# Kernel optimization log

Hardware: AMD Instinct MI355X
Metric: run time of the kernel (lower is better)

## Reference

```python
import jax, jax.numpy as jnp
import numpy as np

MIN_EXPERT_CAPACITY = 4
EPS = 1e-9
CAPACITY_FACTOR = 2.0  # eval capacity factor


def cumsum_exclusive(t, axis):
    return jnp.cumsum(t, axis=axis) - t


def safe_one_hot(idx, depth):
    # one_hot with an extra slot so idx == depth maps to nothing, then slice
    return jax.nn.one_hot(idx, depth + 1)[..., :depth]


def setup_inputs() -> dict:
    key = jax.random.key(0)
    k_x, k_g, k_w1, k_w2 = jax.random.split(key, 4)
    b, n, d, e, h = 2, 4096, 512, 16, 2048
    x = jax.random.normal(k_x, (b, n, d), dtype=jnp.float32)
    w_gating = jax.random.normal(k_g, (d, e), dtype=jnp.float32) / np.sqrt(d)
    w1 = jax.random.normal(k_w1, (e, d, h), dtype=jnp.float32) / np.sqrt(d)
    w2 = jax.random.normal(k_w2, (e, h, d), dtype=jnp.float32) / np.sqrt(h)
    return {"x": x, "w_gating": w_gating, "w1": w1, "w2": w2}


def top2_gating(x, w_gating):
    b, n, d = x.shape
    e = w_gating.shape[-1]
    raw_gates = jax.nn.softmax(jnp.einsum('bnd,de->bne', x, w_gating), axis=-1)

    gate_1 = jnp.max(raw_gates, axis=-1)
    index_1 = jnp.argmax(raw_gates, axis=-1)
    mask_1 = jax.nn.one_hot(index_1, e, dtype=raw_gates.dtype)

    gates_without_top1 = raw_gates * (1.0 - mask_1)
    gate_2 = jnp.max(gates_without_top1, axis=-1)
    index_2 = jnp.argmax(gates_without_top1, axis=-1)
    mask_2 = jax.nn.one_hot(index_2, e, dtype=raw_gates.dtype)

    denom = gate_1 + gate_2 + EPS
    gate_1 = gate_1 / denom
    gate_2 = gate_2 / denom

    # load-balancing loss
    density_1 = jnp.mean(mask_1, axis=-2)
    density_1_proxy = jnp.mean(raw_gates, axis=-2)
    loss = jnp.mean(density_1_proxy * density_1) * float(e * e)

    # second policy == 'all' -> keep mask_2 as-is

    capacity = max(min(n, int((n * 2) * CAPACITY_FACTOR / e)), MIN_EXPERT_CAPACITY)
    cap_f = float(capacity)

    pos1 = cumsum_exclusive(mask_1, axis=-2) * mask_1  # [b,n,e]
    mask_1 = mask_1 * (pos1 < cap_f).astype(mask_1.dtype)
    mask_1_count = jnp.sum(mask_1, axis=-2, keepdims=True)
    mask_1_flat = jnp.sum(mask_1, axis=-1)  # [b,n]
    pos1 = jnp.sum(pos1, axis=-1)
    gate_1 = gate_1 * mask_1_flat

    pos2 = (cumsum_exclusive(mask_2, axis=-2) + mask_1_count) * mask_2
    mask_2 = mask_2 * (pos2 < cap_f).astype(mask_2.dtype)
    mask_2_flat = jnp.sum(mask_2, axis=-1)
    pos2 = jnp.sum(pos2, axis=-1)
    gate_2 = gate_2 * mask_2_flat

    # combine tensor: [b, n, e, c]
    combine = (gate_1[..., None, None] * mask_1_flat[..., None, None]
               * jax.nn.one_hot(index_1, e, dtype=x.dtype)[..., None]
               * safe_one_hot(pos1.astype(jnp.int32), capacity)[..., None, :]
               + gate_2[..., None, None] * mask_2_flat[..., None, None]
               * jax.nn.one_hot(index_2, e, dtype=x.dtype)[..., None]
               * safe_one_hot(pos2.astype(jnp.int32), capacity)[..., None, :])
    dispatch = (combine > 0).astype(combine.dtype)
    return dispatch, combine, loss


def reference(x, w_gating, w1, w2):
    dispatch, combine, loss = top2_gating(x, w_gating)
    # dispatch: gather tokens into expert buckets [e, b, c, d]
    expert_inputs = jnp.einsum('bnd,bnec->ebcd', x, dispatch)
    # expert FFN (eval mode: dropout is identity)
    hidden = jax.nn.relu(jnp.einsum('ebcd,edh->ebch', expert_inputs, w1))
    expert_outputs = jnp.einsum('ebch,ehd->ebcd', hidden, w2)
    # combine back to token order, weighted by gate values
    output = jnp.einsum('ebcd,bnec->bnd', expert_outputs, combine)
    return output
```

## Files before the change

### kernel.cpp

```cpp
#include <hip/hip_runtime.h>

#define BB 2
#define NN 4096
#define DD 512
#define EE 16
#define HH 2048
#define CAP 1024
#define NTOK (BB*NN)
#define MM (BB*CAP)
#define MAXSTRIP 160

typedef unsigned short ushort_t;
typedef __attribute__((ext_vector_type(8))) short bf16x8;
typedef __attribute__((ext_vector_type(4))) float floatx4;

__device__ __forceinline__ ushort_t f2bf(float f) {
    union { float f; unsigned u; } v; v.f = f;
    unsigned r = v.u + 0x7fffu + ((v.u >> 16) & 1u);
    return (ushort_t)(r >> 16);
}

__device__ __forceinline__ void cp16(const void* g, void* l) {
    __builtin_amdgcn_global_load_lds(
        (const __attribute__((address_space(1))) void*)g,
        (__attribute__((address_space(3))) void*)l, 16, 0, 0);
}

__launch_bounds__(256)
__global__ void gating_kernel(const float* __restrict__ x,
                              const float* __restrict__ wg,
                              int* __restrict__ e1, int* __restrict__ e2,
                              float* __restrict__ g1, float* __restrict__ g2,
                              ushort_t* __restrict__ xbf) {
    int wave = threadIdx.x >> 6;
    int lane = threadIdx.x & 63;
    int t = blockIdx.x * 4 + wave;
    const float* xp = x + (size_t)t * DD;

    float4 xa = ((const float4*)xp)[lane * 2];
    float4 xb = ((const float4*)xp)[lane * 2 + 1];
    float xs[8] = {xa.x, xa.y, xa.z, xa.w, xb.x, xb.y, xb.z, xb.w};

    ushort4 h0, h1;
    h0.x = f2bf(xs[0]); h0.y = f2bf(xs[1]); h0.z = f2bf(xs[2]); h0.w = f2bf(xs[3]);
    h1.x = f2bf(xs[4]); h1.y = f2bf(xs[5]); h1.z = f2bf(xs[6]); h1.w = f2bf(xs[7]);
    ushort4* xo = (ushort4*)(xbf + (size_t)t * DD);
    xo[lane * 2] = h0; xo[lane * 2 + 1] = h1;

    float acc[EE];
#pragma unroll
    for (int e = 0; e < EE; e++) acc[e] = 0.f;
    int d0 = lane * 8;
#pragma unroll
    for (int j = 0; j < 8; j++) {
        const float* wrow = wg + (d0 + j) * EE;
#pragma unroll
        for (int e = 0; e < EE; e++) acc[e] = fmaf(xs[j], wrow[e], acc[e]);
    }
#pragma unroll
    for (int off = 32; off > 0; off >>= 1) {
#pragma unroll
        for (int e = 0; e < EE; e++) acc[e] += __shfl_xor(acc[e], off, 64);
    }
    if (lane == 0) {
        float m = acc[0];
#pragma unroll
        for (int e = 1; e < EE; e++) m = fmaxf(m, acc[e]);
        float p[EE]; float s = 0.f;
#pragma unroll
        for (int e = 0; e < EE; e++) { p[e] = __expf(acc[e] - m); s += p[e]; }
        float inv = 1.f / s;
#pragma unroll
        for (int e = 0; e < EE; e++) p[e] *= inv;
        int i1 = 0; float v1 = p[0];
#pragma unroll
        for (int e = 1; e < EE; e++) if (p[e] > v1) { v1 = p[e]; i1 = e; }
        int i2 = (i1 == 0) ? 1 : 0; float v2 = p[i2];
#pragma unroll
        for (int e = 0; e < EE; e++)
            if (e != i1 && p[e] > v2) { v2 = p[e]; i2 = e; }
        float denom = v1 + v2 + 1e-9f;
        e1[t] = i1; e2[t] = i2;
        g1[t] = v1 / denom; g2[t] = v2 / denom;
    }
}

__launch_bounds__(256)
__global__ void scan_kernel(const int* __restrict__ e1, const int* __restrict__ e2,
                            const float* __restrict__ g1, const float* __restrict__ g2,
                            int* __restrict__ s2t, float* __restrict__ s2g,
                            int* __restrict__ used) {
    int b = blockIdx.x / EE;
    int e = blockIdx.x % EE;
    int tid = threadIdx.x;
    const int base = b * NN;
    int n0 = tid * 16;

    unsigned m1 = 0, m2 = 0;
    int c1 = 0, c2 = 0;
#pragma unroll
    for (int j = 0; j < 16; j++) {
        int n = n0 + j;
        if (e1[base + n] == e) { m1 |= 1u << j; c1++; }
        if (e2[base + n] == e) { m2 |= 1u << j; c2++; }
    }
    __shared__ int s1[256], s2[256];
    __shared__ int s_used;
    s1[tid] = c1; s2[tid] = c2;
    __syncthreads();
    for (int off = 1; off < 256; off <<= 1) {
        int a1 = (tid >= off) ? s1[tid - off] : 0;
        int a2 = (tid >= off) ? s2[tid - off] : 0;
        __syncthreads();
        s1[tid] += a1; s2[tid] += a2;
        __syncthreads();
    }
    int total1 = s1[255];
    int total2 = s2[255];
    int kept1 = min(total1, CAP);
    int ex1 = s1[tid] - c1;
    int ex2 = s2[tid] - c2 + kept1;
    const int sbase = (e * BB + b) * CAP;
#pragma unroll
    for (int j = 0; j < 16; j++) {
        int n = n0 + j;
        if (m1 & (1u << j)) {
            if (ex1 < CAP) { s2t[sbase + ex1] = base + n; s2g[sbase + ex1] = g1[base + n]; }
            ex1++;
        }
        if (m2 & (1u << j)) {
            if (ex2 < CAP) { s2t[sbase + ex2] = base + n; s2g[sbase + ex2] = g2[base + n]; }
            ex2++;
        }
    }
    if (tid == 255) {
        int kept2 = min(total2, max(0, CAP - kept1));
        int u = kept1 + kept2;
        used[e * BB + b] = u;
        s_used = u;
    }
    __syncthreads();
    for (int i = s_used + tid; i < CAP; i += 256) s2t[sbase + i] = -1;
}

__global__ void schedule_kernel(const int* __restrict__ used, int* __restrict__ meta) {
    __shared__ int ns[32], pre[32];
    int i = threadIdx.x;
    if (i < 32) {
        int e = i >> 1, b = i & 1;
        ns[i] = (used[e * BB + b] + 127) >> 7;
    }
    __syncthreads();
    if (i == 0) {
        int acc = 0;
        for (int j = 0; j < 32; j++) { pre[j] = acc; acc += ns[j]; }
    }
    __syncthreads();
    if (i < 16) {
        int e = i;
        int xcd = e & 7;
        int mine  = ns[2 * e] + ns[2 * e + 1];
        int po    = (e < 8) ? (e + 8) : (e - 8);
        int other = ns[2 * po] + ns[2 * po + 1];
        if (e < 8) {
            meta[xcd]     = (mine + other) * 16;
            meta[8 + xcd] = (mine + other) * 4;
        }
        int off = (e < 8) ? 0 : other;
        int* sc1 = meta + 16 + xcd * 512 + off * 16;
        int j = 0;
        for (int col = 0; col < 16; col++)
            for (int bb = 0; bb < 2; bb++)
                for (int s = 0; s < ns[2 * e + bb]; s++) {
                    int wi = pre[2 * e + bb] + s;
                    sc1[j++] = (e << 17) | (wi << 9) | ((bb * 8 + s) << 5) | col;
                }
        int* sc2 = meta + 16 + 4096 + xcd * 128 + off * 4;
        j = 0;
        for (int col = 0; col < 4; col++)
            for (int bb = 0; bb < 2; bb++)
                for (int s = 0; s < ns[2 * e + bb]; s++) {
                    int wi = pre[2 * e + bb] + s;
                    sc2[j++] = (e << 17) | (wi << 9) | ((bb * 8 + s) << 5) | col;
                }
    }
}

__global__ void transpose_bf16(const float* __restrict__ in,
                               ushort_t* __restrict__ outp, int R, int C) {
    __shared__ float tile[32][33];
    const float* slab = in + (size_t)blockIdx.z * R * C;
    ushort_t* oslab = outp + (size_t)blockIdx.z * R * C;
    int c0 = blockIdx.x * 32, r0 = blockIdx.y * 32;
    int tx = threadIdx.x, ty = threadIdx.y;
#pragma unroll
    for (int j = 0; j < 4; j++)
        tile[ty + j * 8][tx] = slab[(size_t)(r0 + ty + j * 8) * C + c0 + tx];
    __syncthreads();
#pragma unroll
    for (int j = 0; j < 4; j++)
        oslab[(size_t)(c0 + ty + j * 8) * R + r0 + tx] = f2bf(tile[tx][ty + j * 8]);
}

template <int MODE>
__launch_bounds__(256)
__global__ void gemm_mfma(const ushort_t* __restrict__ Abase,
                          const ushort_t* __restrict__ Bt,
                          void* __restrict__ Cout,
                          const int* __restrict__ meta,
                          const int* __restrict__ s2t,
                          const float* __restrict__ s2g) {
    constexpr int K = (MODE == 0) ? DD : HH;
    constexpr int KITERS = K / 32;

    int xcd = blockIdx.x;
    if ((int)blockIdx.y >= meta[(MODE == 0 ? 0 : 8) + xcd]) return;
    int job = meta[16 + (MODE == 0 ? 0 : 4096) + xcd * (MODE == 0 ? 512 : 128) + blockIdx.y];
    int col0  = (job & 31) * 128;
    int ytile = (job >> 5) & 15;
    int wi    = (job >> 9) & 255;
    int e     = job >> 17;

    __shared__ ushort_t As[2][128 * 32];
    __shared__ ushort_t Bs[2][128 * 32];

    int tid = threadIdx.x;
    int lane = tid & 63;
    int wid = tid >> 6;
    int wave_m = (wid & 1) << 6;
    int wave_n = (wid >> 1) << 6;
    int lm = lane & 15;
    int quad = lane >> 4;
    int sw = (quad ^ ((lm >> 1) & 3)) * 8;

    const ushort_t* ga[2];
    const ushort_t* gb[2];
#pragma unroll
    for (int it = 0; it < 2; it++) {
        int idx = it * 256 + tid;
        int r = idx >> 2;
        int cg = (idx & 3) ^ ((r >> 1) & 3);
        if (MODE == 0) {
            int tok = s2t[e * MM + ytile * 128 + r];
            if (tok < 0) tok = 0;
            ga[it] = Abase + (size_t)tok * DD + cg * 8;
        } else {
            ga[it] = Abase + (size_t)(wi * 128 + r) * HH + cg * 8;
        }
        gb[it] = Bt + (size_t)e * HH * DD + (size_t)(col0 + r) * K + cg * 8;
    }

    auto stage = [&](int buf, int ki) {
#pragma unroll
        for (int it = 0; it < 2; it++)
            cp16(ga[it] + ki * 32, &As[buf][(it * 256 + tid) * 8]);
#pragma unroll
        for (int it = 0; it < 2; it++)
            cp16(gb[it] + ki * 32, &Bs[buf][(it * 256 + tid) * 8]);
    };

    floatx4 acc[4][4];
#pragma unroll
    for (int i = 0; i < 4; i++)
#pragma unroll
        for (int j = 0; j < 4; j++)
            acc[i][j] = (floatx4)(0.f);

    stage(0, 0);
#pragma unroll 2
    for (int ki = 0; ki < KITERS; ki++) {
        int cur = ki & 1;
        if (ki + 1 < KITERS) {
            stage(cur ^ 1, ki + 1);
            asm volatile("s_waitcnt vmcnt(4)\ns_barrier" ::: "memory");
        } else {
            asm volatile("s_waitcnt vmcnt(0)\ns_barrier" ::: "memory");
        }
        bf16x8 af[4], bfr[4];
#pragma unroll
        for (int mt = 0; mt < 4; mt++)
            af[mt] = *(const bf16x8*)&As[cur][(wave_m + mt * 16 + lm) * 32 + sw];
#pragma unroll
        for (int nt = 0; nt < 4; nt++)
            bfr[nt] = *(const bf16x8*)&Bs[cur][(wave_n + nt * 16 + lm) * 32 + sw];
#pragma unroll
        for (int mt = 0; mt < 4; mt++)
#pragma unroll
            for (int nt = 0; nt < 4; nt++)
                acc[mt][nt] = __builtin_amdgcn_mfma_f32_16x16x32_bf16(
                    af[mt], bfr[nt], acc[mt][nt], 0, 0, 0);
        asm volatile("s_waitcnt lgkmcnt(0)\ns_barrier" ::: "memory");
    }

    if (MODE == 0) {
        ushort_t* hp = (ushort_t*)Cout + (size_t)wi * 128 * HH;
#pragma unroll
        for (int mt = 0; mt < 4; mt++) {
#pragma unroll
            for (int r = 0; r < 4; r++) {
                int row = wave_m + mt * 16 + quad * 4 + r;
#pragma unroll
                for (int nt = 0; nt < 4; nt++) {
                    int col = col0 + wave_n + nt * 16 + lm;
                    hp[(size_t)row * HH + col] = f2bf(fmaxf(acc[mt][nt][r], 0.f));
                }
            }
        }
    } else {
        float* outp = (float*)Cout;
#pragma unroll
        for (int mt = 0; mt < 4; mt++) {
#pragma unroll
            for (int r = 0; r < 4; r++) {
                int row = wave_m + mt * 16 + quad * 4 + r;
                int slot = e * MM + ytile * 128 + row;
                int tok = s2t[slot];
                if (tok < 0) continue;
                float g = s2g[slot];
#pragma unroll
                for (int nt = 0; nt < 4; nt++) {
                    int col = col0 + wave_n + nt * 16 + lm;
                    atomicAdd(outp + (size_t)tok * DD + col, g * acc[mt][nt][r]);
                }
            }
        }
    }
}

extern "C" void kernel_launch(void* const* d_in, const int* in_sizes, int n_in,
                              void* d_out, int out_size, void* d_ws, size_t ws_size,
                              hipStream_t stream) {
    const float* x  = (const float*)d_in[0];
    const float* wg = (const float*)d_in[1];
    const float* w1 = (const float*)d_in[2];
    const float* w2 = (const float*)d_in[3];
    float* out = (float*)d_out;

    char* ws = (char*)d_ws;
    int*      e1   = (int*)(ws);
    int*      e2   = (int*)(ws + 32768);
    float*    g1   = (float*)(ws + 65536);
    float*    g2   = (float*)(ws + 98304);
    int*      used = (int*)(ws + 131072);
    int*      meta = (int*)(ws + 132096);
    int*      s2t  = (int*)(ws + 152704);
    float*    s2g  = (float*)(ws + 283776);
    ushort_t* xbf  = (ushort_t*)(ws + 414848);
    ushort_t* wt   = (ushort_t*)(ws + 8803456);
    ushort_t* hid  = (ushort_t*)(ws + 42357888);

    hipMemsetAsync(out, 0, (size_t)NTOK * DD * sizeof(float), stream);

    gating_kernel<<<NTOK / 4, 256, 0, stream>>>(x, wg, e1, e2, g1, g2, xbf);
    scan_kernel<<<BB * EE, 256, 0, stream>>>(e1, e2, g1, g2, s2t, s2g, used);
    schedule_kernel<<<1, 64, 0, stream>>>(used, meta);

    transpose_bf16<<<dim3(HH / 32, DD / 32, EE), dim3(32, 8), 0, stream>>>(w1, wt, DD, HH);
    gemm_mfma<0><<<dim3(8, 512), 256, 0, stream>>>(xbf, wt, hid, meta, s2t, s2g);

    transpose_bf16<<<dim3(DD / 32, HH / 32, EE), dim3(32, 8), 0, stream>>>(w2, wt, HH, DD);
    gemm_mfma<1><<<dim3(8, 128), 256, 0, stream>>>(hid, wt, out, meta, s2t, s2g);
}
```

Before: 368.0 us.

## Triple-buffer LDS tiles in expert GEMM to prefetch two k-steps ahead

Moves the expert GEMM main loop from double to triple buffering of the A and B LDS tiles, issuing global-to-LDS loads two k-iterations ahead with adjusted vmcnt waits. The loop is unrolled by three with constant buffer indices, and the second barrier now comes right after the LDS fragment reads, before the MFMAs, so the next stage can overwrite that buffer while compute runs. The goal is to hide more global memory latency. In exchange LDS use per block grows to 48KB, which may lower occupancy, and there are still two barriers per k-step.

Measured after the change: 355.6 us. 3.4% less time.

```diff
diff --git a/kernel.cpp b/kernel.cpp
--- a/kernel.cpp
+++ b/kernel.cpp
@@ -221,8 +221,8 @@
     int wi    = (job >> 9) & 255;
     int e     = job >> 17;
 
-    __shared__ ushort_t As[2][128 * 32];
-    __shared__ ushort_t Bs[2][128 * 32];
+    __shared__ ushort_t As[3][128 * 32];
+    __shared__ ushort_t Bs[3][128 * 32];
 
     int tid = threadIdx.x;
     int lane = tid & 63;
@@ -267,30 +267,41 @@
             acc[i][j] = (floatx4)(0.f);
 
     stage(0, 0);
-#pragma unroll 2
-    for (int ki = 0; ki < KITERS; ki++) {
-        int cur = ki & 1;
-        if (ki + 1 < KITERS) {
-            stage(cur ^ 1, ki + 1);
-            asm volatile("s_waitcnt vmcnt(4)\ns_barrier" ::: "memory");
-        } else {
-            asm volatile("s_waitcnt vmcnt(0)\ns_barrier" ::: "memory");
-        }
-        bf16x8 af[4], bfr[4];
-#pragma unroll
-        for (int mt = 0; mt < 4; mt++)
-            af[mt] = *(const bf16x8*)&As[cur][(wave_m + mt * 16 + lm) * 32 + sw];
-#pragma unroll
-        for (int nt = 0; nt < 4; nt++)
-            bfr[nt] = *(const bf16x8*)&Bs[cur][(wave_n + nt * 16 + lm) * 32 + sw];
-#pragma unroll
-        for (int mt = 0; mt < 4; mt++)
-#pragma unroll
-            for (int nt = 0; nt < 4; nt++)
-                acc[mt][nt] = __builtin_amdgcn_mfma_f32_16x16x32_bf16(
-                    af[mt], bfr[nt], acc[mt][nt], 0, 0, 0);
-        asm volatile("s_waitcnt lgkmcnt(0)\ns_barrier" ::: "memory");
-    }
+    stage(1, 1);
+
+#define KSTEP(CUR, NXT, KI)                                                     \
+    do {                                                                        \
+        int ki_ = (KI);                                                         \
+        if (ki_ + 2 < KITERS) {                                                 \
+            stage(NXT, ki_ + 2);                                                \
+            asm volatile("s_waitcnt vmcnt(8)\ns_barrier" ::: "memory");         \
+        } else if (ki_ + 2 == KITERS) {                                         \
+            asm volatile("s_waitcnt vmcnt(4)\ns_barrier" ::: "memory");         \
+        } else {                                                                \
+            asm volatile("s_waitcnt vmcnt(0)\ns_barrier" ::: "memory");         \
+        }                                                                       \
+        bf16x8 af[4], bfr[4];                                                   \
+        _Pragma("unroll")                                                       \
+        for (int mt = 0; mt < 4; mt++)                                          \
+            af[mt] = *(const bf16x8*)&As[CUR][(wave_m + mt * 16 + lm) * 32 + sw]; \
+        _Pragma("unroll")                                                       \
+        for (int nt = 0; nt < 4; nt++)                                          \
+            bfr[nt] = *(const bf16x8*)&Bs[CUR][(wave_n + nt * 16 + lm) * 32 + sw]; \
+        asm volatile("s_waitcnt lgkmcnt(0)\ns_barrier" ::: "memory");           \
+        _Pragma("unroll")                                                       \
+        for (int mt = 0; mt < 4; mt++)                                          \
+            _Pragma("unroll")                                                   \
+            for (int nt = 0; nt < 4; nt++)                                      \
+                acc[mt][nt] = __builtin_amdgcn_mfma_f32_16x16x32_bf16(          \
+                    af[mt], bfr[nt], acc[mt][nt], 0, 0, 0);                     \
+    } while (0)
+
+    for (int kb = 0; kb < KITERS; kb += 3) {
+        KSTEP(0, 2, kb);
+        if (kb + 1 < KITERS) KSTEP(1, 0, kb + 1);
+        if (kb + 2 < KITERS) KSTEP(2, 1, kb + 2);
+    }
+#undef KSTEP
 
     if (MODE == 0) {
         ushort_t* hp = (ushort_t*)Cout + (size_t)wi * 128 * HH;
```

## Enlarge expert GEMM tiles to 256x256 with 512 threads and split-K second GEMM

Applied to the files above, without the earlier changes.

Both expert GEMMs move from 128x128 tiles with a 32-wide K step to 256x256 tiles with a 64-wide K step, run by 512 threads. Each thread now holds an 8x4 MFMA accumulator grid, and the LDS swizzle is adjusted to match. The second GEMM splits K into two halves across jobs, relying on the existing atomic adds to combine the partial sums. The scheduler is rewritten for 256-row strips. The aim is more reuse per global load and fewer barriers per FLOP. In exchange it needs 128KB of LDS per block, more registers and fewer blocks, which lowers occupancy and load balance, and it pads token strips more coarsely.

Result: slower. 403.1 us (+9.5%).

```diff
diff --git a/kernel.cpp b/kernel.cpp
--- a/kernel.cpp
+++ b/kernel.cpp
@@ -8,7 +8,7 @@
 #define CAP 1024
 #define NTOK (BB*NN)
 #define MM (BB*CAP)
-#define MAXSTRIP 160
+#define MAXSTRIP 96
 
 typedef unsigned short ushort_t;
 typedef __attribute__((ext_vector_type(8))) short bf16x8;
@@ -148,7 +148,7 @@
     int i = threadIdx.x;
     if (i < 32) {
         int e = i >> 1, b = i & 1;
-        ns[i] = (used[e * BB + b] + 127) >> 7;
+        ns[i] = (used[e * BB + b] + 255) >> 8;
     }
     __syncthreads();
     if (i == 0) {
@@ -163,25 +163,25 @@
         int po    = (e < 8) ? (e + 8) : (e - 8);
         int other = ns[2 * po] + ns[2 * po + 1];
         if (e < 8) {
-            meta[xcd]     = (mine + other) * 16;
+            meta[xcd]     = (mine + other) * 8;
             meta[8 + xcd] = (mine + other) * 4;
         }
         int off = (e < 8) ? 0 : other;
-        int* sc1 = meta + 16 + xcd * 512 + off * 16;
+        int* sc1 = meta + 16 + xcd * 512 + off * 8;
         int j = 0;
-        for (int col = 0; col < 16; col++)
+        for (int col = 0; col < 8; col++)
             for (int bb = 0; bb < 2; bb++)
                 for (int s = 0; s < ns[2 * e + bb]; s++) {
                     int wi = pre[2 * e + bb] + s;
-                    sc1[j++] = (e << 17) | (wi << 9) | ((bb * 8 + s) << 5) | col;
+                    sc1[j++] = (e << 17) | (wi << 9) | ((bb * 4 + s) << 5) | col;
                 }
         int* sc2 = meta + 16 + 4096 + xcd * 128 + off * 4;
         j = 0;
-        for (int col = 0; col < 4; col++)
+        for (int c = 0; c < 4; c++)
             for (int bb = 0; bb < 2; bb++)
                 for (int s = 0; s < ns[2 * e + bb]; s++) {
                     int wi = pre[2 * e + bb] + s;
-                    sc2[j++] = (e << 17) | (wi << 9) | ((bb * 8 + s) << 5) | col;
+                    sc2[j++] = (e << 17) | (wi << 9) | ((bb * 4 + s) << 5) | c;
                 }
     }
 }
@@ -203,99 +203,117 @@
 }
 
 template <int MODE>
-__launch_bounds__(256)
+__launch_bounds__(512)
 __global__ void gemm_mfma(const ushort_t* __restrict__ Abase,
                           const ushort_t* __restrict__ Bt,
                           void* __restrict__ Cout,
                           const int* __restrict__ meta,
                           const int* __restrict__ s2t,
                           const float* __restrict__ s2g) {
-    constexpr int K = (MODE == 0) ? DD : HH;
-    constexpr int KITERS = K / 32;
+    constexpr int BROW = (MODE == 0) ? DD : HH;
+    constexpr int KJOB = (MODE == 0) ? DD : (HH / 2);
+    constexpr int KITERS = KJOB / 64;
 
     int xcd = blockIdx.x;
     if ((int)blockIdx.y >= meta[(MODE == 0 ? 0 : 8) + xcd]) return;
     int job = meta[16 + (MODE == 0 ? 0 : 4096) + xcd * (MODE == 0 ? 512 : 128) + blockIdx.y];
-    int col0  = (job & 31) * 128;
+    int c     = job & 31;
     int ytile = (job >> 5) & 15;
     int wi    = (job >> 9) & 255;
     int e     = job >> 17;
-
-    __shared__ ushort_t As[2][128 * 32];
-    __shared__ ushort_t Bs[2][128 * 32];
+    int col0  = (MODE == 0) ? c * 256 : (c >> 1) * 256;
+    int koff  = (MODE == 0) ? 0 : (c & 1) * (HH / 2);
+
+    __shared__ ushort_t As[2][256 * 64];
+    __shared__ ushort_t Bs[2][256 * 64];
 
     int tid = threadIdx.x;
     int lane = tid & 63;
     int wid = tid >> 6;
-    int wave_m = (wid & 1) << 6;
-    int wave_n = (wid >> 1) << 6;
+    int wave_m = (wid & 1) * 128;
+    int wave_n = (wid >> 1) * 64;
     int lm = lane & 15;
     int quad = lane >> 4;
-    int sw = (quad ^ ((lm >> 1) & 3)) * 8;
-
-    const ushort_t* ga[2];
-    const ushort_t* gb[2];
-#pragma unroll
-    for (int it = 0; it < 2; it++) {
-        int idx = it * 256 + tid;
-        int r = idx >> 2;
-        int cg = (idx & 3) ^ ((r >> 1) & 3);
+
+    const ushort_t* gaP[4];
+    const ushort_t* gbP[4];
+#pragma unroll
+    for (int it = 0; it < 4; it++) {
+        int p = it * 512 + tid;
+        int r = p >> 3;
+        int cg = (p & 7) ^ (r & 7);
         if (MODE == 0) {
-            int tok = s2t[e * MM + ytile * 128 + r];
+            int tok = s2t[e * MM + ytile * 256 + r];
             if (tok < 0) tok = 0;
-            ga[it] = Abase + (size_t)tok * DD + cg * 8;
+            gaP[it] = Abase + (size_t)tok * DD + cg * 8;
         } else {
-            ga[it] = Abase + (size_t)(wi * 128 + r) * HH + cg * 8;
-        }
-        gb[it] = Bt + (size_t)e * HH * DD + (size_t)(col0 + r) * K + cg * 8;
-    }
-
-    auto stage = [&](int buf, int ki) {
-#pragma unroll
-        for (int it = 0; it < 2; it++)
-            cp16(ga[it] + ki * 32, &As[buf][(it * 256 + tid) * 8]);
-#pragma unroll
-        for (int it = 0; it < 2; it++)
-            cp16(gb[it] + ki * 32, &Bs[buf][(it * 256 + tid) * 8]);
+            gaP[it] = Abase + (size_t)(wi * 256 + r) * HH + koff + cg * 8;
+        }
+        gbP[it] = Bt + (size_t)e * HH * DD + (size_t)(col0 + r) * BROW
+                  + (MODE == 0 ? 0 : koff) + cg * 8;
+    }
+
+    auto stage = [&](int buf, int kt) {
+#pragma unroll
+        for (int it = 0; it < 4; it++)
+            cp16(gaP[it] + kt * 64, &As[buf][(it * 512 + tid) * 8]);
+#pragma unroll
+        for (int it = 0; it < 4; it++)
+            cp16(gbP[it] + kt * 64, &Bs[buf][(it * 512 + tid) * 8]);
     };
 
-    floatx4 acc[4][4];
-#pragma unroll
-    for (int i = 0; i < 4; i++)
+    floatx4 acc[8][4];
+#pragma unroll
+    for (int i = 0; i < 8; i++)
 #pragma unroll
         for (int j = 0; j < 4; j++)
             acc[i][j] = (floatx4)(0.f);
 
+    int sw0 = (quad ^ (lm & 7)) * 8;
+    int sw1 = ((4 + quad) ^ (lm & 7)) * 8;
+
     stage(0, 0);
 #pragma unroll 2
-    for (int ki = 0; ki < KITERS; ki++) {
-        int cur = ki & 1;
-        if (ki + 1 < KITERS) {
-            stage(cur ^ 1, ki + 1);
-            asm volatile("s_waitcnt vmcnt(4)\ns_barrier" ::: "memory");
+    for (int t = 0; t < KITERS; t++) {
+        int cur = t & 1;
+        if (t + 1 < KITERS) {
+            stage(cur ^ 1, t + 1);
+            asm volatile("s_waitcnt vmcnt(8)\ns_barrier" ::: "memory");
         } else {
             asm volatile("s_waitcnt vmcnt(0)\ns_barrier" ::: "memory");
         }
-        bf16x8 af[4], bfr[4];
-#pragma unroll
-        for (int mt = 0; mt < 4; mt++)
-            af[mt] = *(const bf16x8*)&As[cur][(wave_m + mt * 16 + lm) * 32 + sw];
+        bf16x8 af[8], bfr[4];
+#pragma unroll
+        for (int mt = 0; mt < 8; mt++)
+            af[mt] = *(const bf16x8*)&As[cur][(wave_m + mt * 16 + lm) * 64 + sw0];
 #pragma unroll
         for (int nt = 0; nt < 4; nt++)
-            bfr[nt] = *(const bf16x8*)&Bs[cur][(wave_n + nt * 16 + lm) * 32 + sw];
-#pragma unroll
-        for (int mt = 0; mt < 4; mt++)
+            bfr[nt] = *(const bf16x8*)&Bs[cur][(wave_n + nt * 16 + lm) * 64 + sw0];
+#pragma unroll
+        for (int mt = 0; mt < 8; mt++)
 #pragma unroll
             for (int nt = 0; nt < 4; nt++)
                 acc[mt][nt] = __builtin_amdgcn_mfma_f32_16x16x32_bf16(
                     af[mt], bfr[nt], acc[mt][nt], 0, 0, 0);
+#pragma unroll
+        for (int mt = 0; mt < 8; mt++)
+            af[mt] = *(const bf16x8*)&As[cur][(wave_m + mt * 16 + lm) * 64 + sw1];
+#pragma unroll
+        for (int nt = 0; nt < 4; nt++)
+            bfr[nt] = *(const bf16x8*)&Bs[cur][(wave_n + nt * 16 + lm) * 64 + sw1];
         asm volatile("s_waitcnt lgkmcnt(0)\ns_barrier" ::: "memory");
+#pragma unroll
+        for (int mt = 0; mt < 8; mt++)
+#pragma unroll
+            for (int nt = 0; nt < 4; nt++)
+                acc[mt][nt] = __builtin_amdgcn_mfma_f32_16x16x32_bf16(
+                    af[mt], bfr[nt], acc[mt][nt], 0, 0, 0);
     }
 
     if (MODE == 0) {
-        ushort_t* hp = (ushort_t*)Cout + (size_t)wi * 128 * HH;
-#pragma unroll
-        for (int mt = 0; mt < 4; mt++) {
+        ushort_t* hp = (ushort_t*)Cout + (size_t)wi * 256 * HH;
+#pragma unroll
+        for (int mt = 0; mt < 8; mt++) {
 #pragma unroll
             for (int r = 0; r < 4; r++) {
                 int row = wave_m + mt * 16 + quad * 4 + r;
@@ -309,11 +327,11 @@
     } else {
         float* outp = (float*)Cout;
 #pragma unroll
-        for (int mt = 0; mt < 4; mt++) {
+        for (int mt = 0; mt < 8; mt++) {
 #pragma unroll
             for (int r = 0; r < 4; r++) {
                 int row = wave_m + mt * 16 + quad * 4 + r;
-                int slot = e * MM + ytile * 128 + row;
+                int slot = e * MM + ytile * 256 + row;
                 int tok = s2t[slot];
                 if (tok < 0) continue;
                 float g = s2g[slot];
@@ -356,8 +374,8 @@
     schedule_kernel<<<1, 64, 0, stream>>>(used, meta);
 
     transpose_bf16<<<dim3(HH / 32, DD / 32, EE), dim3(32, 8), 0, stream>>>(w1, wt, DD, HH);
-    gemm_mfma<0><<<dim3(8, 512), 256, 0, stream>>>(xbf, wt, hid, meta, s2t, s2g);
+    gemm_mfma<0><<<dim3(8, 128), 512, 0, stream>>>(xbf, wt, hid, meta, s2t, s2g);
 
     transpose_bf16<<<dim3(DD / 32, HH / 32, EE), dim3(32, 8), 0, stream>>>(w2, wt, HH, DD);
-    gemm_mfma<1><<<dim3(8, 128), 256, 0, stream>>>(hid, wt, out, meta, s2t, s2g);
-}
+    gemm_mfma<1><<<dim3(8, 64), 512, 0, stream>>>(hid, wt, out, meta, s2t, s2g);
+}
```
